# Performance work log

Measured on AMD Instinct MI355X. Metric: run time of the kernel, lower is better.

The kernel has to match this reference:

```python
import jax, jax.numpy as jnp
import numpy as np

EPS = 1e-7
PI = np.pi


def _vel_to_R(vel):
    # vel: [..., 3] -> rotation matrix [..., 3, 3] (ZY convention from spherical angles)
    rho = jnp.linalg.norm(vel, axis=-1, keepdims=True)
    theta = jnp.arctan2(vel[..., 1:2], vel[..., 0:1])
    theta = theta + (theta < 0).astype(theta.dtype) * (2.0 * PI)  # symmetric_theta=False
    phi = jnp.arccos(jnp.clip(vel[..., 2:3] / (rho + EPS), -1.0, 1.0))
    ct, st = jnp.cos(theta)[..., 0], jnp.sin(theta)[..., 0]
    cp, sp = jnp.cos(phi)[..., 0], jnp.sin(phi)[..., 0]
    z = jnp.zeros_like(ct)
    R = jnp.stack([
        jnp.stack([cp * ct, -st, sp * ct], -1),
        jnp.stack([cp * st, ct, sp * st], -1),
        jnp.stack([-sp, z, cp], -1),
    ], -2)
    return R


def _rotate(R, x):
    return jnp.einsum('...ij,...j->...i', R, x)


def setup_inputs() -> dict:
    key = jax.random.key(0)
    B, N, H, D = 128, 100, 128, 3
    in_size = 2 * D  # 6
    nef = 3 * D + D * (D - 1) // 2 + in_size  # 18 edge features
    ks = jax.random.split(key, 12)

    inputs = jax.random.normal(ks[0], (B, N, in_size), jnp.float32)

    # fully connected edges (no self loops)
    send_np, recv_np = np.nonzero(~np.eye(N, dtype=bool))
    send_edges = jnp.asarray(send_np, jnp.int32)
    recv_edges = jnp.asarray(recv_np, jnp.int32)

    def lin(k, fin, fout):
        return jax.random.normal(k, (fin, fout), jnp.float32) / np.sqrt(fin)

    return dict(
        inputs=inputs,
        W1=lin(ks[1], nef, H), b1=jnp.zeros((H,), jnp.float32),
        W2=lin(ks[2], H, H), b2=jnp.zeros((H,), jnp.float32),
        Wr=lin(ks[3], in_size, H), br=jnp.zeros((H,), jnp.float32),
        W3=lin(ks[4], H, H), b3=jnp.zeros((H,), jnp.float32),
        W4=lin(ks[5], H, H), b4=jnp.zeros((H,), jnp.float32),
        W5=lin(ks[6], H, in_size), b5=jnp.zeros((in_size,), jnp.float32),
        send_edges=send_edges, recv_edges=recv_edges,
    )


def reference(inputs, W1, b1, W2, b2, Wr, br, W3, b3, W4, b4, W5, b5,
              send_edges, recv_edges):
    D = 3
    B, N, _ = inputs.shape

    # ---- Localizer.canonicalize_inputs ----
    vel = inputs[..., D:2 * D]
    Rnode = _vel_to_R(vel)                       # [B,N,3,3]
    Rinv_node = jnp.swapaxes(Rnode, -1, -2)
    canon_vel = _rotate(Rinv_node, vel)
    rel_feat = jnp.concatenate([jnp.zeros_like(canon_vel), canon_vel], -1)  # [B,N,6]

    # ---- Localizer.create_edge_attr ----
    x_j = inputs[:, send_edges]                  # [B,E,6] senders
    x_i = inputs[:, recv_edges]                  # [B,E,6] receivers
    R = _vel_to_R(x_i[..., D:2 * D])
    R_inv = jnp.swapaxes(R, -1, -2)
    rel_pos = x_j[..., :D] - x_i[..., :D]
    rot_rel = _rotate(R_inv, rel_pos)
    send_R = _vel_to_R(x_j[..., D:2 * D])
    rot_or = R_inv @ send_R
    euler = jnp.stack([
        jnp.arctan2(rot_or[..., 1, 0], rot_or[..., 0, 0]),
        jnp.arcsin(-rot_or[..., 2, 0]),
        jnp.arctan2(rot_or[..., 2, 1], rot_or[..., 2, 2]),
    ], -1) / PI
    dist = jnp.linalg.norm(rel_pos, axis=-1, keepdims=True)
    rho_e = jnp.linalg.norm(rot_rel, axis=-1, keepdims=True)
    theta_e = jnp.arctan2(rot_rel[..., 1:2], rot_rel[..., 0:1])  # symmetric theta
    phi_e = jnp.arccos(jnp.clip(rot_rel[..., 2:3] / (rho_e + EPS), -1.0, 1.0))
    rot_vel = _rotate(R_inv, x_j[..., D:2 * D])
    edge_attr = jnp.concatenate(
        [rot_rel, euler, dist, theta_e, phi_e, rot_vel], -1)   # [B,E,12]
    edge_attr = jnp.concatenate([edge_attr, rel_feat[:, recv_edges]], -1)  # [B,E,18]

    # ---- GNN: edge MLP + scatter-mean + out MLP (dropout off in eval) ----
    h = jax.nn.silu(edge_attr @ W1 + b1) @ W2 + b2               # [B,E,H]
    agg = jnp.zeros((B, N, h.shape[-1]), h.dtype).at[:, recv_edges].add(h)
    cnt = jnp.zeros((N,), h.dtype).at[recv_edges].add(1.0)
    agg = agg / jnp.maximum(cnt, 1.0)[None, :, None]             # scatter mean
    aug = agg + rel_feat @ Wr + br
    p = jax.nn.relu(aug @ W3 + b3)
    p = jax.nn.relu(p @ W4 + b4)
    pred = p @ W5 + b5                                           # [B,N,6]

    # ---- Globalizer: rotate each 3-vector chunk back to global frame ----
    gl = jnp.concatenate(
        [_rotate(Rnode, pred[..., i:i + D]) for i in range(0, pred.shape[-1], D)], -1)
    return inputs + gl
```

## Files before the change

### kernel.cpp

```cpp
#include <hip/hip_runtime.h>
#include <math.h>

#define EPSF 1e-7f
constexpr int NN  = 100;
constexpr int DEG = 99;
constexpr int IN  = 6;
constexpr int H   = 128;
constexpr int G   = 4;
constexpr float INV_PI = 0.3183098861837907f;
constexpr float LOG2E  = 1.4426950408889634f;
constexpr float LN2    = 0.6931471805599453f;

typedef __attribute__((ext_vector_type(4))) _Float16 half4;
typedef __attribute__((ext_vector_type(8))) _Float16 half8;
typedef __attribute__((ext_vector_type(4))) float f32x4;

constexpr int XST = 144;
constexpr int SXS = 15;
constexpr int TS  = 50;
constexpr int NT  = 25;

__device__ __forceinline__ float clampf(float x, float lo, float hi) {
    return fminf(fmaxf(x, lo), hi);
}
__device__ __forceinline__ float sig2(float y) {
    return __builtin_amdgcn_rcpf(1.f + __builtin_amdgcn_exp2f(-y));
}
__device__ __forceinline__ float fast_atan2(float y, float x) {
    float ax = fabsf(x), ay = fabsf(y);
    float mx = fmaxf(ax, ay), mn = fminf(ax, ay);
    float r = mn * __builtin_amdgcn_rcpf(fmaxf(mx, 1e-35f));
    float r2 = r * r;
    float p = fmaf(r2, -0.0851330f, 0.1801410f);
    p = fmaf(r2, p, -0.3302995f);
    p = fmaf(r2, p, 0.9998660f);
    float t = r * p;
    t = (ay > ax) ? (1.5707963267948966f - t) : t;
    t = (x < 0.f) ? (3.14159265358979323f - t) : t;
    return copysignf(t, y);
}
__device__ __forceinline__ float fast_asin(float z) {
    return fast_atan2(z, sqrtf(fmaxf(0.f, (1.f - z) * (1.f + z))));
}
__device__ __forceinline__ float fast_acos(float z) {
    return fast_atan2(sqrtf(fmaxf(0.f, (1.f - z) * (1.f + z))), z);
}
__device__ __forceinline__ void vel_to_R(float vx, float vy, float vz, float* R) {
    float rho = sqrtf(vx * vx + vy * vy + vz * vz);
    float rxy = sqrtf(vx * vx + vy * vy);
    float inv = __builtin_amdgcn_rcpf(rxy);
    bool big = rxy > 1e-30f;
    float ct = big ? vx * inv : 1.f;
    float st = big ? vy * inv : 0.f;
    float cp = clampf(vz * __builtin_amdgcn_rcpf(rho + EPSF), -1.f, 1.f);
    float sp = sqrtf(fmaxf(0.f, 1.f - cp * cp));
    R[0] = cp * ct; R[1] = -st; R[2] = sp * ct;
    R[3] = cp * st; R[4] = ct;  R[5] = sp * st;
    R[6] = -sp;     R[7] = 0.f; R[8] = cp;
}

__global__ void conv_w(const float* __restrict__ W1, const float* __restrict__ W2,
                       const float* __restrict__ W3, const float* __restrict__ W4,
                       half4* __restrict__ w1f, half8* __restrict__ wmlp) {
    int t = blockIdx.x * blockDim.x + threadIdx.x;
    if (t >= 104 * 64) return;
    int L = t & 63, f = t >> 6;
    int m = L & 15, qd = L >> 4;
    if (f < 8) {
        int n = f * 16 + m;
        half4 v;
#pragma unroll
        for (int j = 0; j < 4; ++j) {
            int k = qd * 4 + j;
            v[j] = (k < 12) ? (_Float16)(W1[k * H + n] * LOG2E) : (_Float16)0.f;
        }
        w1f[f * 64 + L] = v;
    } else {
        int ff = f - 8;
        int layer = ff >> 5, rest = ff & 31;
        int kt = rest >> 3, nt = rest & 7;
        const float* W = (layer == 0) ? W2 : (layer == 1) ? W3 : W4;
        float scale = (layer == 0) ? LN2 : 1.f;
        int n = nt * 16 + m;
        half8 v;
#pragma unroll
        for (int j = 0; j < 8; ++j)
            v[j] = (_Float16)(W[(kt * 32 + qd * 8 + j) * H + n] * scale);
        wmlp[((layer * 4 + kt) * 8 + nt) * 64 + L] = v;
    }
}

__global__ __launch_bounds__(256, 8)
void locs_fused(const float* __restrict__ in,
                const float* __restrict__ W1, const float* __restrict__ b1,
                const float* __restrict__ b2,
                const float* __restrict__ Wr, const float* __restrict__ br,
                const float* __restrict__ b3, const float* __restrict__ b4,
                const float* __restrict__ W5, const float* __restrict__ b5,
                const half4* __restrict__ w1f, const half8* __restrict__ wmlp,
                float* __restrict__ out) {
    __shared__ _Float16 hpool[NT * TS * 4];
    __shared__ float sxr[NN * SXS];
    __shared__ float cvF[16];
    __shared__ float pbF[G * 96];
    __shared__ float predF[G * 8];

    const int tid = threadIdx.x;
    const int L   = tid & 63;
    const int wv  = tid >> 6;
    const int q   = L >> 4;
    const int lm  = L & 15;
    const int bn0 = blockIdx.x * G;
    const int bB  = bn0 / NN;
    const int n0  = bn0 - bB * NN;

    _Float16* xh0 = hpool;
    _Float16* xh1 = hpool + 4 * XST;

    {
        half4 z = {0, 0, 0, 0};
        for (int i = tid; i < NT * TS; i += 256) *(half4*)&hpool[i * 4] = z;
    }
    if (tid < NN) {
        const float* xi = in + (bB * NN + tid) * IN;
        float R[9];
        float px = xi[0], py = xi[1], pz = xi[2];
        float vx = xi[3], vy = xi[4], vz = xi[5];
        vel_to_R(vx, vy, vz, R);
        float* dst = sxr + tid * SXS;
#pragma unroll
        for (int k = 0; k < 9; ++k) dst[k] = R[k];
        dst[9] = px; dst[10] = py; dst[11] = pz;
        dst[12] = vx; dst[13] = vy; dst[14] = vz;
        int g = tid - n0;
        if ((unsigned)g < (unsigned)G) {
            cvF[g * 4 + 0] = R[0] * vx + R[3] * vy + R[6] * vz;
            cvF[g * 4 + 1] = R[1] * vx + R[4] * vy + R[7] * vz;
            cvF[g * 4 + 2] = R[2] * vx + R[5] * vy + R[8] * vz;
        }
    }
    __syncthreads();

    float bs[2];
    {
        float cv0 = cvF[q * 4 + 0], cv1 = cvF[q * 4 + 1], cv2 = cvF[q * 4 + 2];
#pragma unroll
        for (int i = 0; i < 2; ++i) {
            int ch = wv * 32 + i * 16 + lm;
            bs[i] = (b1[ch] + cv0 * W1[15 * H + ch] + cv1 * W1[16 * H + ch]
                   + cv2 * W1[17 * H + ch]) * LOG2E;
        }
    }
    half4 bfr[2];
#pragma unroll
    for (int i = 0; i < 2; ++i) bfr[i] = w1f[(wv * 2 + i) * 64 + L];

#pragma unroll
    for (int rnd = 0; rnd < 2; ++rnd) {
        int j = tid + rnd * 256;
        if (j < G * DEG) {
            int g = j / DEG;
            int e = j - g * DEG;
            int nG = n0 + g;
            int s = e < nG ? e : e + 1;
            const float* rn = sxr + nG * SXS;
            const float* rs = sxr + s * SXS;
            float Rn[9];
#pragma unroll
            for (int k = 0; k < 9; ++k) Rn[k] = rn[k];
            float rel0 = rs[9] - rn[9], rel1 = rs[10] - rn[10], rel2 = rs[11] - rn[11];
            float vjx = rs[12], vjy = rs[13], vjz = rs[14];
            float Rs0 = rs[0], Rs1 = rs[1], Rs2 = rs[2];
            float Rs3 = rs[3], Rs4 = rs[4], Rs5 = rs[5];
            float Rs6 = rs[6], Rs7 = rs[7], Rs8 = rs[8];
            float rr0 = Rn[0] * rel0 + Rn[3] * rel1 + Rn[6] * rel2;
            float rr1 = Rn[1] * rel0 + Rn[4] * rel1 + Rn[7] * rel2;
            float rr2 = Rn[2] * rel0 + Rn[5] * rel1 + Rn[8] * rel2;
            float ro00 = Rn[0] * Rs0 + Rn[3] * Rs3 + Rn[6] * Rs6;
            float ro10 = Rn[1] * Rs0 + Rn[4] * Rs3 + Rn[7] * Rs6;
            float ro20 = Rn[2] * Rs0 + Rn[5] * Rs3 + Rn[8] * Rs6;
            float ro21 = Rn[2] * Rs1 + Rn[5] * Rs4 + Rn[8] * Rs7;
            float ro22 = Rn[2] * Rs2 + Rn[5] * Rs5 + Rn[8] * Rs8;
            float dist = sqrtf(rel0 * rel0 + rel1 * rel1 + rel2 * rel2);
            half4 f0, f1, f2;
            f0[0] = (_Float16)rr0; f0[1] = (_Float16)rr1; f0[2] = (_Float16)rr2;
            f0[3] = (_Float16)(fast_atan2(ro10, ro00) * INV_PI);
            f1[0] = (_Float16)(fast_asin(clampf(-ro20, -1.f, 1.f)) * INV_PI);
            f1[1] = (_Float16)(fast_atan2(ro21, ro22) * INV_PI);
            f1[2] = (_Float16)dist;
            f1[3] = (_Float16)fast_atan2(rr1, rr0);
            f2[0] = (_Float16)fast_acos(clampf(rr2 * __builtin_amdgcn_rcpf(dist + EPSF), -1.f, 1.f));
            f2[1] = (_Float16)(Rn[0] * vjx + Rn[3] * vjy + Rn[6] * vjz);
            f2[2] = (_Float16)(Rn[1] * vjx + Rn[4] * vjy + Rn[7] * vjz);
            f2[3] = (_Float16)(Rn[2] * vjx + Rn[5] * vjy + Rn[8] * vjz);
            int t = e >> 2;
            int mrow = g * 4 + (e & 3);
            _Float16* dst = hpool + (t * TS + mrow) * 4;
            *(half4*)(dst +   0)      = f0;
            *(half4*)(dst + 16 * 4)   = f1;
            *(half4*)(dst + 32 * 4)   = f2;
        }
    }
    __syncthreads();

    {
        float part[2] = {0.f, 0.f};
        f32x4 c[2];
#pragma unroll
        for (int i = 0; i < 2; ++i) c[i] = (f32x4){bs[i], bs[i], bs[i], bs[i]};
        const int loff = (q < 3) ? (q * 16 + lm) : 48;
        half4 a_cur = *(const half4*)&hpool[(0 * TS + loff) * 4];
#pragma unroll
        for (int t = 0; t < NT; ++t) {
            half4 a_next;
            if (t < NT - 1) a_next = *(const half4*)&hpool[((t + 1) * TS + loff) * 4];
            f32x4 d0 = __builtin_amdgcn_mfma_f32_16x16x16f16(a_cur, bfr[0], c[0], 0, 0, 0);
            f32x4 d1 = __builtin_amdgcn_mfma_f32_16x16x16f16(a_cur, bfr[1], c[1], 0, 0, 0);
#pragma unroll
            for (int r = 0; r < 4; ++r) {
                part[0] += d0[r] * sig2(d0[r]);
                part[1] += d1[r] * sig2(d1[r]);
            }
            a_cur = a_next;
        }
        __syncthreads();
#pragma unroll
        for (int i = 0; i < 2; ++i)
            xh0[q * XST + wv * 32 + i * 16 + lm] =
                (_Float16)(part[i] - bs[i] * sig2(bs[i]));
    }
    __syncthreads();

#pragma unroll
    for (int layer = 0; layer < 3; ++layer) {
        const _Float16* src = (layer & 1) ? xh1 : xh0;
        _Float16*       dst = (layer & 1) ? xh0 : xh1;
        half8 bh[8];
#pragma unroll
        for (int kt = 0; kt < 4; ++kt) {
            int base = ((layer * 4 + kt) * 8 + wv * 2) * 64 + L;
#pragma unroll
            for (int i = 0; i < 2; ++i) bh[kt * 2 + i] = wmlp[base + i * 64];
        }
        int rowb = (lm & 3) * XST;
        half8 ah[4];
#pragma unroll
        for (int kt = 0; kt < 4; ++kt)
            ah[kt] = *(const half8*)&src[rowb + kt * 32 + q * 8];
        f32x4 acc[2];
#pragma unroll
        for (int i = 0; i < 2; ++i) acc[i] = (f32x4){0.f, 0.f, 0.f, 0.f};
#pragma unroll
        for (int kt = 0; kt < 4; ++kt)
#pragma unroll
            for (int i = 0; i < 2; ++i)
                acc[i] = __builtin_amdgcn_mfma_f32_16x16x32_f16(ah[kt], bh[kt * 2 + i],
                                                                acc[i], 0, 0, 0);
        if (L < 16) {
#pragma unroll
            for (int i = 0; i < 2; ++i) {
                int ch = (wv * 2 + i) * 16 + lm;
                if (layer == 0) {
                    float b2c = b2[ch], brc = br[ch];
                    float w3c = Wr[3 * H + ch], w4c = Wr[4 * H + ch], w5c = Wr[5 * H + ch];
#pragma unroll
                    for (int r = 0; r < 4; ++r)
                        dst[r * XST + ch] = (_Float16)(acc[i][r] * (1.f / 99.f) + b2c
                                          + cvF[r * 4 + 0] * w3c + cvF[r * 4 + 1] * w4c
                                          + cvF[r * 4 + 2] * w5c + brc);
                } else {
                    float bb = (layer == 1) ? b3[ch] : b4[ch];
#pragma unroll
                    for (int r = 0; r < 4; ++r)
                        dst[r * XST + ch] = (_Float16)fmaxf(0.f, acc[i][r] + bb);
                }
            }
        }
        __syncthreads();
    }

    if (tid < 96) {
        int o = tid >> 4, sl = tid & 15, kb = sl * 8;
        float w5[8];
#pragma unroll
        for (int j = 0; j < 8; ++j) w5[j] = W5[(kb + j) * IN + o];
#pragma unroll
        for (int g = 0; g < G; ++g) {
            half8 xv = *(const half8*)&xh1[g * XST + kb];
            float s = 0.f;
#pragma unroll
            for (int j = 0; j < 8; ++j) s = fmaf((float)xv[j], w5[j], s);
            pbF[g * 96 + sl * 6 + o] = s;
        }
    }
    __syncthreads();
    if (tid < 24) {
        int g = tid / 6, o = tid - g * 6;
        float s = b5[o];
#pragma unroll
        for (int sl = 0; sl < 16; ++sl) s += pbF[g * 96 + sl * 6 + o];
        predF[g * 8 + o] = s;
    }
    __syncthreads();
    if (tid < 24) {
        int g = tid / 6, o = tid - g * 6;
        int r = (o < 3) ? o : o - 3;
        int off = (o < 3) ? 0 : 3;
        const float* Rg = sxr + (n0 + g) * SXS;
        float gl = Rg[r * 3 + 0] * predF[g * 8 + off + 0]
                 + Rg[r * 3 + 1] * predF[g * 8 + off + 1]
                 + Rg[r * 3 + 2] * predF[g * 8 + off + 2];
        int bng = bn0 + g;
        out[bng * IN + o] = Rg[9 + o] + gl;
    }
}

extern "C" void kernel_launch(void* const* d_in, const int* in_sizes, int n_in,
                              void* d_out, int out_size, void* d_ws, size_t ws_size,
                              hipStream_t stream) {
    const float* in = (const float*)d_in[0];
    const float* W1 = (const float*)d_in[1];
    const float* b1 = (const float*)d_in[2];
    const float* W2 = (const float*)d_in[3];
    const float* b2 = (const float*)d_in[4];
    const float* Wr = (const float*)d_in[5];
    const float* br = (const float*)d_in[6];
    const float* W3 = (const float*)d_in[7];
    const float* b3 = (const float*)d_in[8];
    const float* W4 = (const float*)d_in[9];
    const float* b4 = (const float*)d_in[10];
    const float* W5 = (const float*)d_in[11];
    const float* b5 = (const float*)d_in[12];
    float* out = (float*)d_out;

    half4* w1f  = (half4*)d_ws;
    half8* wmlp = (half8*)((char*)d_ws + 4096);

    const int BN = in_sizes[0] / IN;
    conv_w<<<26, 256, 0, stream>>>(W1, W2, W3, W4, w1f, wmlp);
    locs_fused<<<BN / G, 256, 0, stream>>>(in, W1, b1, b2, Wr, br, b3, b4,
                                           W5, b5, w1f, wmlp, out);
}
```

Before: 128.1 us.

## Process eight nodes per block with 512 threads, one channel tile per wave

Each block now handles 8 receiver nodes, up from 4, using 512 threads across 8 waves. Each wave owns one 16-channel tile and runs two 25-step MFMA groups, and the MLP layers use all 16 MFMA rows. This halves the per-node cost of building the 100-node rotation table in shared memory and of the fixed setup, and it fills the MFMA row dimension that was half empty. In exchange the grid becomes 13 blocks per graph with a partial last block, the block uses more shared memory, and occupancy per CU may drop.

```diff
diff --git a/kernel.cpp b/kernel.cpp
--- a/kernel.cpp
+++ b/kernel.cpp
@@ -6,7 +6,8 @@
 constexpr int DEG = 99;
 constexpr int IN  = 6;
 constexpr int H   = 128;
-constexpr int G   = 4;
+constexpr int G   = 8;
+constexpr int BPG = 13;
 constexpr float INV_PI = 0.3183098861837907f;
 constexpr float LOG2E  = 1.4426950408889634f;
 constexpr float LN2    = 0.6931471805599453f;
@@ -18,7 +19,7 @@
 constexpr int XST = 144;
 constexpr int SXS = 15;
 constexpr int TS  = 50;
-constexpr int NT  = 25;
+constexpr int NT  = 50;
 
 __device__ __forceinline__ float clampf(float x, float lo, float hi) {
     return fminf(fmaxf(x, lo), hi);
@@ -90,7 +91,7 @@
     }
 }
 
-__global__ __launch_bounds__(256, 8)
+__global__ __launch_bounds__(512, 8)
 void locs_fused(const float* __restrict__ in,
                 const float* __restrict__ W1, const float* __restrict__ b1,
                 const float* __restrict__ b2,
@@ -101,7 +102,7 @@
                 float* __restrict__ out) {
     __shared__ _Float16 hpool[NT * TS * 4];
     __shared__ float sxr[NN * SXS];
-    __shared__ float cvF[16];
+    __shared__ float cvF[32];
     __shared__ float pbF[G * 96];
     __shared__ float predF[G * 8];
 
@@ -110,17 +111,19 @@
     const int wv  = tid >> 6;
     const int q   = L >> 4;
     const int lm  = L & 15;
-    const int bn0 = blockIdx.x * G;
-    const int bB  = bn0 / NN;
-    const int n0  = bn0 - bB * NN;
+    const int bB   = blockIdx.x / BPG;
+    const int blkg = blockIdx.x - bB * BPG;
+    const int n0   = blkg * G;
+    const int cnt  = (NN - n0 < G) ? (NN - n0) : G;
 
     _Float16* xh0 = hpool;
-    _Float16* xh1 = hpool + 4 * XST;
+    _Float16* xh1 = hpool + G * XST;
 
     {
         half4 z = {0, 0, 0, 0};
-        for (int i = tid; i < NT * TS; i += 256) *(half4*)&hpool[i * 4] = z;
-    }
+        for (int i = tid; i < NT * TS; i += 512) *(half4*)&hpool[i * 4] = z;
+    }
+    if (tid >= cnt * 4 && tid < 32) cvF[tid] = 0.f;
     if (tid < NN) {
         const float* xi = in + (bB * NN + tid) * IN;
         float R[9];
@@ -133,7 +136,7 @@
         dst[9] = px; dst[10] = py; dst[11] = pz;
         dst[12] = vx; dst[13] = vy; dst[14] = vz;
         int g = tid - n0;
-        if ((unsigned)g < (unsigned)G) {
+        if ((unsigned)g < (unsigned)cnt) {
             cvF[g * 4 + 0] = R[0] * vx + R[3] * vy + R[6] * vz;
             cvF[g * 4 + 1] = R[1] * vx + R[4] * vy + R[7] * vz;
             cvF[g * 4 + 2] = R[2] * vx + R[5] * vy + R[8] * vz;
@@ -141,24 +144,22 @@
     }
     __syncthreads();
 
-    float bs[2];
+    float bsA, bsB;
     {
-        float cv0 = cvF[q * 4 + 0], cv1 = cvF[q * 4 + 1], cv2 = cvF[q * 4 + 2];
-#pragma unroll
-        for (int i = 0; i < 2; ++i) {
-            int ch = wv * 32 + i * 16 + lm;
-            bs[i] = (b1[ch] + cv0 * W1[15 * H + ch] + cv1 * W1[16 * H + ch]
-                   + cv2 * W1[17 * H + ch]) * LOG2E;
-        }
-    }
-    half4 bfr[2];
-#pragma unroll
-    for (int i = 0; i < 2; ++i) bfr[i] = w1f[(wv * 2 + i) * 64 + L];
+        int ch = wv * 16 + lm;
+        float w15 = W1[15 * H + ch], w16 = W1[16 * H + ch], w17 = W1[17 * H + ch];
+        float bb = b1[ch];
+        bsA = (bb + cvF[q * 4 + 0] * w15 + cvF[q * 4 + 1] * w16
+             + cvF[q * 4 + 2] * w17) * LOG2E;
+        bsB = (bb + cvF[(q + 4) * 4 + 0] * w15 + cvF[(q + 4) * 4 + 1] * w16
+             + cvF[(q + 4) * 4 + 2] * w17) * LOG2E;
+    }
+    half4 bfr = w1f[wv * 64 + L];
 
 #pragma unroll
     for (int rnd = 0; rnd < 2; ++rnd) {
-        int j = tid + rnd * 256;
-        if (j < G * DEG) {
+        int j = tid + rnd * 512;
+        if (j < cnt * DEG) {
             int g = j / DEG;
             int e = j - g * DEG;
             int nG = n0 + g;
@@ -193,8 +194,8 @@
             f2[1] = (_Float16)(Rn[0] * vjx + Rn[3] * vjy + Rn[6] * vjz);
             f2[2] = (_Float16)(Rn[1] * vjx + Rn[4] * vjy + Rn[7] * vjz);
             f2[3] = (_Float16)(Rn[2] * vjx + Rn[5] * vjy + Rn[8] * vjz);
-            int t = e >> 2;
-            int mrow = g * 4 + (e & 3);
+            int t = (e >> 2) + (g >> 2) * 25;
+            int mrow = (g & 3) * 4 + (e & 3);
             _Float16* dst = hpool + (t * TS + mrow) * 4;
             *(half4*)(dst +   0)      = f0;
             *(half4*)(dst + 16 * 4)   = f1;
@@ -205,29 +206,27 @@
 
     {
         float part[2] = {0.f, 0.f};
-        f32x4 c[2];
-#pragma unroll
-        for (int i = 0; i < 2; ++i) c[i] = (f32x4){bs[i], bs[i], bs[i], bs[i]};
+        const float bsv[2] = {bsA, bsB};
         const int loff = (q < 3) ? (q * 16 + lm) : 48;
-        half4 a_cur = *(const half4*)&hpool[(0 * TS + loff) * 4];
-#pragma unroll
-        for (int t = 0; t < NT; ++t) {
-            half4 a_next;
-            if (t < NT - 1) a_next = *(const half4*)&hpool[((t + 1) * TS + loff) * 4];
-            f32x4 d0 = __builtin_amdgcn_mfma_f32_16x16x16f16(a_cur, bfr[0], c[0], 0, 0, 0);
-            f32x4 d1 = __builtin_amdgcn_mfma_f32_16x16x16f16(a_cur, bfr[1], c[1], 0, 0, 0);
-#pragma unroll
-            for (int r = 0; r < 4; ++r) {
-                part[0] += d0[r] * sig2(d0[r]);
-                part[1] += d1[r] * sig2(d1[r]);
+#pragma unroll
+        for (int grp = 0; grp < 2; ++grp) {
+            f32x4 c = (f32x4){bsv[grp], bsv[grp], bsv[grp], bsv[grp]};
+            const int tb = grp * 25;
+            half4 a_cur = *(const half4*)&hpool[(tb * TS + loff) * 4];
+#pragma unroll
+            for (int t = 0; t < 25; ++t) {
+                half4 a_next;
+                if (t < 24) a_next = *(const half4*)&hpool[((tb + t + 1) * TS + loff) * 4];
+                f32x4 d = __builtin_amdgcn_mfma_f32_16x16x16f16(a_cur, bfr, c, 0, 0, 0);
+#pragma unroll
+                for (int r = 0; r < 4; ++r) part[grp] += d[r] * sig2(d[r]);
+                a_cur = a_next;
             }
-            a_cur = a_next;
         }
         __syncthreads();
-#pragma unroll
-        for (int i = 0; i < 2; ++i)
-            xh0[q * XST + wv * 32 + i * 16 + lm] =
-                (_Float16)(part[i] - bs[i] * sig2(bs[i]));
+        int ch = wv * 16 + lm;
+        xh0[q * XST + ch]       = (_Float16)(part[0] - bsA * sig2(bsA));
+        xh0[(q + 4) * XST + ch] = (_Float16)(part[1] - bsB * sig2(bsB));
     }
     __syncthreads();
 
@@ -235,44 +234,37 @@
     for (int layer = 0; layer < 3; ++layer) {
         const _Float16* src = (layer & 1) ? xh1 : xh0;
         _Float16*       dst = (layer & 1) ? xh0 : xh1;
-        half8 bh[8];
-#pragma unroll
-        for (int kt = 0; kt < 4; ++kt) {
-            int base = ((layer * 4 + kt) * 8 + wv * 2) * 64 + L;
-#pragma unroll
-            for (int i = 0; i < 2; ++i) bh[kt * 2 + i] = wmlp[base + i * 64];
-        }
-        int rowb = (lm & 3) * XST;
+        half8 bh[4];
+#pragma unroll
+        for (int kt = 0; kt < 4; ++kt)
+            bh[kt] = wmlp[((layer * 4 + kt) * 8 + wv) * 64 + L];
+        int rowb = (lm & 7) * XST;
         half8 ah[4];
 #pragma unroll
         for (int kt = 0; kt < 4; ++kt)
             ah[kt] = *(const half8*)&src[rowb + kt * 32 + q * 8];
-        f32x4 acc[2];
-#pragma unroll
-        for (int i = 0; i < 2; ++i) acc[i] = (f32x4){0.f, 0.f, 0.f, 0.f};
+        f32x4 acc = (f32x4){0.f, 0.f, 0.f, 0.f};
 #pragma unroll
         for (int kt = 0; kt < 4; ++kt)
-#pragma unroll
-            for (int i = 0; i < 2; ++i)
-                acc[i] = __builtin_amdgcn_mfma_f32_16x16x32_f16(ah[kt], bh[kt * 2 + i],
-                                                                acc[i], 0, 0, 0);
-        if (L < 16) {
-#pragma unroll
-            for (int i = 0; i < 2; ++i) {
-                int ch = (wv * 2 + i) * 16 + lm;
-                if (layer == 0) {
-                    float b2c = b2[ch], brc = br[ch];
-                    float w3c = Wr[3 * H + ch], w4c = Wr[4 * H + ch], w5c = Wr[5 * H + ch];
-#pragma unroll
-                    for (int r = 0; r < 4; ++r)
-                        dst[r * XST + ch] = (_Float16)(acc[i][r] * (1.f / 99.f) + b2c
-                                          + cvF[r * 4 + 0] * w3c + cvF[r * 4 + 1] * w4c
-                                          + cvF[r * 4 + 2] * w5c + brc);
-                } else {
-                    float bb = (layer == 1) ? b3[ch] : b4[ch];
-#pragma unroll
-                    for (int r = 0; r < 4; ++r)
-                        dst[r * XST + ch] = (_Float16)fmaxf(0.f, acc[i][r] + bb);
+            acc = __builtin_amdgcn_mfma_f32_16x16x32_f16(ah[kt], bh[kt], acc, 0, 0, 0);
+        if (L < 32) {
+            int ch = wv * 16 + lm;
+            if (layer == 0) {
+                float b2c = b2[ch], brc = br[ch];
+                float w3c = Wr[3 * H + ch], w4c = Wr[4 * H + ch], w5c = Wr[5 * H + ch];
+#pragma unroll
+                for (int r = 0; r < 4; ++r) {
+                    int rr = q * 4 + r;
+                    dst[rr * XST + ch] = (_Float16)(acc[r] * (1.f / 99.f) + b2c
+                                      + cvF[rr * 4 + 0] * w3c + cvF[rr * 4 + 1] * w4c
+                                      + cvF[rr * 4 + 2] * w5c + brc);
+                }
+            } else {
+                float bb = (layer == 1) ? b3[ch] : b4[ch];
+#pragma unroll
+                for (int r = 0; r < 4; ++r) {
+                    int rr = q * 4 + r;
+                    dst[rr * XST + ch] = (_Float16)fmaxf(0.f, acc[r] + bb);
                 }
             }
         }
@@ -294,7 +286,7 @@
         }
     }
     __syncthreads();
-    if (tid < 24) {
+    if (tid < 48) {
         int g = tid / 6, o = tid - g * 6;
         float s = b5[o];
 #pragma unroll
@@ -302,16 +294,18 @@
         predF[g * 8 + o] = s;
     }
     __syncthreads();
-    if (tid < 24) {
+    if (tid < 48) {
         int g = tid / 6, o = tid - g * 6;
-        int r = (o < 3) ? o : o - 3;
-        int off = (o < 3) ? 0 : 3;
-        const float* Rg = sxr + (n0 + g) * SXS;
-        float gl = Rg[r * 3 + 0] * predF[g * 8 + off + 0]
-                 + Rg[r * 3 + 1] * predF[g * 8 + off + 1]
-                 + Rg[r * 3 + 2] * predF[g * 8 + off + 2];
-        int bng = bn0 + g;
-        out[bng * IN + o] = Rg[9 + o] + gl;
+        if (g < cnt) {
+            int r = (o < 3) ? o : o - 3;
+            int off = (o < 3) ? 0 : 3;
+            const float* Rg = sxr + (n0 + g) * SXS;
+            float gl = Rg[r * 3 + 0] * predF[g * 8 + off + 0]
+                     + Rg[r * 3 + 1] * predF[g * 8 + off + 1]
+                     + Rg[r * 3 + 2] * predF[g * 8 + off + 2];
+            int bng = bB * NN + n0 + g;
+            out[bng * IN + o] = Rg[9 + o] + gl;
+        }
     }
 }
 
@@ -337,7 +331,8 @@
     half8* wmlp = (half8*)((char*)d_ws + 4096);
 
     const int BN = in_sizes[0] / IN;
+    const int nGraphs = BN / NN;
     conv_w<<<26, 256, 0, stream>>>(W1, W2, W3, W4, w1f, wmlp);
-    locs_fused<<<BN / G, 256, 0, stream>>>(in, W1, b1, b2, Wr, br, b3, b4,
-                                           W5, b5, w1f, wmlp, out);
-}
+    locs_fused<<<nGraphs * BPG, 512, 0, stream>>>(in, W1, b1, b2, Wr, br, b3, b4,
+                                                  W5, b5, w1f, wmlp, out);
+}
```

Measured after the change: 129.0 us. About the same (+0.7%).
